# Kernel optimization log

Hardware: AMD Instinct MI355X
Metric: run time of the kernel (lower is better)

## Reference

```python
import jax, jax.numpy as jnp
import numpy as np

K = 7      # kernel_size
PAD = 3    # padding ('same' with stride 1)
G = 16     # groups


def _unfold(x):
    """torch nn.Unfold equivalent, stride=1, dilation=1.
    Returns [B, C, K*K, H, W] with kernel positions ordered (kh, kw),
    matching torch's (c, kh, kw) channel-major layout after reshape."""
    B, C, H, W = x.shape
    xp = jnp.pad(x, ((0, 0), (0, 0), (PAD, PAD), (PAD, PAD)))
    patches = jnp.stack(
        [xp[:, :, i:i + H, j:j + W] for i in range(K) for j in range(K)],
        axis=2,
    )
    return patches


def setup_inputs() -> dict:
    key = jax.random.key(0)
    k1, k2, k3 = jax.random.split(key, 3)
    B, C, H, W = 4, 256, 64, 64
    x = jax.random.normal(k1, (B, C, H, W), dtype=jnp.float32)
    # 1x1 conv producing kernel_prod*groups = 49*16 = 784 channels (with bias)
    w_kernel = jax.random.normal(k2, (G * K * K, C), dtype=jnp.float32) * 0.05
    b_kernel = jax.random.normal(k3, (G * K * K,), dtype=jnp.float32) * 0.05
    return {"x": x, "w_kernel": w_kernel, "b_kernel": b_kernel}


def reference(x, w_kernel, b_kernel):
    B, C, H, W = x.shape
    Cg = C // G
    # unfolded input: [B, G, C//G, K*K, H, W]
    patches = _unfold(x).reshape(B, G, Cg, K * K, H, W)
    # dynamic per-pixel kernel: AvgPool(k=1) is identity at stride 1,
    # then 1x1 conv with bias -> [B, G*K*K, H, W]
    kern = jnp.einsum('bchw,kc->bkhw', x, w_kernel) + b_kernel[None, :, None, None]
    kern = kern.reshape(B, G, 1, K * K, H, W)
    # multiply and sum-reduce over kernel positions, flatten groups
    out = (patches * kern).sum(axis=3).reshape(B, C, H, W)
    return out
```

## Files before the change

kernel.cpp:

```cpp
#include <hip/hip_runtime.h>


#define B_   4
#define C_   256
#define G_   16
#define KK_  49
#define KS_  7
#define PD_  3

#define PROW  70
#define POCT  (PROW*PROW)
#define XP8_BYTES (B_*32*POCT*16)
#define WBF_OFF   XP8_BYTES

#define SKW   28

typedef __attribute__((ext_vector_type(8))) short bf16x8;
typedef __attribute__((ext_vector_type(4))) float f32x4;
typedef unsigned short ushort_t;

__device__ inline unsigned f2bf(float f) {
    unsigned u = __float_as_uint(f);
    u += 0x7FFF + ((u >> 16) & 1);
    return u >> 16;
}

__global__ __launch_bounds__(256)
void cvt_xp8(const float* __restrict__ x, const float* __restrict__ wk,
             ushort_t* __restrict__ xp8, unsigned* __restrict__ wbf) {
    const int t = threadIdx.x;
    if (blockIdx.x == 64) {
        const int slice = blockIdx.z * 4 + blockIdx.y;
        const float2* wk2 = (const float2*)wk;
        const int base = slice * 6272;
        for (int k = t; k < 6272; k += 256) {
            float2 v = wk2[base + k];
            wbf[base + k] = f2bf(v.x) | (f2bf(v.y) << 16);
        }
        return;
    }
    if (blockIdx.x == 65) {
        const int b  = blockIdx.z;
        const int o0 = blockIdx.y * 8;
        const uint4 z = make_uint4(0u, 0u, 0u, 0u);
        #pragma unroll
        for (int o = 0; o < 8; ++o) {
            ushort_t* base = xp8 + (size_t)((b << 5) + o0 + o) * POCT * 8;
            for (int e = t; e < 804; e += 256) {
                int row, col;
                if (e < 420) {
                    row = e / 70; col = e - row * 70;
                    if (row >= 3) row += 64;
                } else {
                    int f = e - 420;
                    row = 3 + f / 6;
                    int m = f - (f / 6) * 6;
                    col = (m < 3) ? m : 64 + m;
                }
                *(uint4*)(base + (row * PROW + col) * 8) = z;
            }
        }
        return;
    }
    __shared__ float tile[64][65];
    const int p0 = blockIdx.x * 64;
    const int c0 = blockIdx.y * 64;
    const int b  = blockIdx.z;
    const int px_r = t & 63;
    #pragma unroll
    for (int i = 0; i < 16; ++i) {
        int ch = (t >> 6) + i * 4;
        tile[ch][px_r] = x[((size_t)(b * C_ + c0 + ch) << 12) + p0 + px_r];
    }
    __syncthreads();
    const int px = t & 63;
    const int ob = t >> 6;
    #pragma unroll
    for (int jj = 0; jj < 2; ++jj) {
        const int j = ob + jj * 4;
        unsigned u[4];
        #pragma unroll
        for (int k2 = 0; k2 < 4; ++k2) {
            float a0 = tile[j * 8 + 2 * k2][px];
            float a1 = tile[j * 8 + 2 * k2 + 1][px];
            u[k2] = f2bf(a0) | (f2bf(a1) << 16);
        }
        ushort_t* dst = xp8 + ((size_t)((b << 5) + (c0 >> 3) + j) * POCT
                               + (blockIdx.x + 3) * PROW + 3 + px) * 8;
        *(uint4*)dst = make_uint4(u[0], u[1], u[2], u[3]);
    }
}

__global__ __launch_bounds__(512, 8)
void inv_fused(const ushort_t* __restrict__ xp8,
               const ushort_t* __restrict__ wbf,
               const float* __restrict__ bk,
               float* __restrict__ out) {
    __shared__ unsigned kern2[256 * SKW];

    const int bid  = blockIdx.x;
    const int g    = bid >> 6;
    const int b    = (bid >> 4) & 3;
    const int tile = bid & 15;
    const int gy0  = tile * 4;
    const int p0   = tile * 256;

    const int tid  = threadIdx.x;
    const int wv   = tid >> 6;
    const int ln15 = tid & 15;
    const int quad = (tid & 63) >> 4;

    f32x4 acc[8];
    #pragma unroll
    for (int i = 0; i < 8; ++i) acc[i] = (f32x4){0.f, 0.f, 0.f, 0.f};

    const char* bbase = (const char*)xp8 + (size_t)b * 32 * POCT * 16;
    const char* abase = (const char*)wbf + (size_t)g * KK_ * 512;

    int vb0, vb1;
    {
        int gi0 = p0 + wv * 32 + ln15;
        int gi1 = gi0 + 16;
        vb0 = (quad * POCT + ((gi0 >> 6) + 3) * PROW + 3 + (gi0 & 63)) * 16;
        vb1 = (quad * POCT + ((gi1 >> 6) + 3) * PROW + 3 + (gi1 & 63)) * 16;
    }
    int va  = ln15 * 512 + quad * 16;
    int va3 = 48 * 512 + quad * 16;

    #pragma unroll
    for (int k = 0; k < 8; ++k) {
        bf16x8 af0 = *(const bf16x8*)(abase + va);
        bf16x8 af1 = *(const bf16x8*)(abase + 8192 + va);
        bf16x8 af2 = *(const bf16x8*)(abase + 16384 + va);
        bf16x8 af3 = *(const bf16x8*)(abase + va3);
        bf16x8 bf0 = *(const bf16x8*)(bbase + vb0);
        bf16x8 bf1 = *(const bf16x8*)(bbase + vb1);
        acc[0] = __builtin_amdgcn_mfma_f32_16x16x32_bf16(af0, bf0, acc[0], 0, 0, 0);
        acc[1] = __builtin_amdgcn_mfma_f32_16x16x32_bf16(af0, bf1, acc[1], 0, 0, 0);
        acc[2] = __builtin_amdgcn_mfma_f32_16x16x32_bf16(af1, bf0, acc[2], 0, 0, 0);
        acc[3] = __builtin_amdgcn_mfma_f32_16x16x32_bf16(af1, bf1, acc[3], 0, 0, 0);
        acc[4] = __builtin_amdgcn_mfma_f32_16x16x32_bf16(af2, bf0, acc[4], 0, 0, 0);
        acc[5] = __builtin_amdgcn_mfma_f32_16x16x32_bf16(af2, bf1, acc[5], 0, 0, 0);
        acc[6] = __builtin_amdgcn_mfma_f32_16x16x32_bf16(af3, bf0, acc[6], 0, 0, 0);
        acc[7] = __builtin_amdgcn_mfma_f32_16x16x32_bf16(af3, bf1, acc[7], 0, 0, 0);
        va  += 64;  va3 += 64;
        vb0 += 4 * POCT * 16; vb1 += 4 * POCT * 16;
    }

    #pragma unroll
    for (int mt = 0; mt < 3; ++mt) {
        const int m0 = mt * 16 + quad * 4;
        const float b0 = bk[g * KK_ + m0],     b1 = bk[g * KK_ + m0 + 1];
        const float b2 = bk[g * KK_ + m0 + 2], b3 = bk[g * KK_ + m0 + 3];
        #pragma unroll
        for (int nt = 0; nt < 2; ++nt) {
            const int p = wv * 32 + nt * 16 + ln15;
            uint2 d;
            d.x = f2bf(acc[mt * 2 + nt][0] + b0) | (f2bf(acc[mt * 2 + nt][1] + b1) << 16);
            d.y = f2bf(acc[mt * 2 + nt][2] + b2) | (f2bf(acc[mt * 2 + nt][3] + b3) << 16);
            *(uint2*)&kern2[p * SKW + mt * 8 + quad * 2] = d;
        }
    }
    if (quad == 0) {
        const float b48 = bk[g * KK_ + 48];
        #pragma unroll
        for (int nt = 0; nt < 2; ++nt) {
            const int p = wv * 32 + nt * 16 + ln15;
            kern2[p * SKW + 24] = f2bf(acc[6 + nt][0] + b48);
        }
    }

    __syncthreads();

    const int pix = tid & 255;
    const int ho  = tid >> 8;
    unsigned kd[28];
    {
        const uint4* kr = (const uint4*)&kern2[pix * SKW];
        #pragma unroll
        for (int q = 0; q < 7; ++q) {
            uint4 h = kr[q];
            kd[4*q] = h.x; kd[4*q+1] = h.y; kd[4*q+2] = h.z; kd[4*q+3] = h.w;
        }
    }

    const int py = pix >> 6, px = pix & 63;
    int vh = ((2 * g + ho) * POCT + (gy0 + py) * PROW + px) * 16;

    float a[8];
    #pragma unroll
    for (int q = 0; q < 8; ++q) a[q] = 0.f;
    #pragma unroll
    for (int kh = 0; kh < KS_; ++kh) {
        #pragma unroll
        for (int kw = 0; kw < KS_; ++kw) {
            uint4 hv = *(const uint4*)(bbase + vh + kw * 16);
            const int t49 = kh * KS_ + kw;
            unsigned d = kd[t49 >> 1];
            float kk = __uint_as_float((t49 & 1) ? (d & 0xffff0000u) : (d << 16));
            a[0] = fmaf(__uint_as_float(hv.x << 16), kk, a[0]);
            a[1] = fmaf(__uint_as_float(hv.x),       kk, a[1]);
            a[2] = fmaf(__uint_as_float(hv.y << 16), kk, a[2]);
            a[3] = fmaf(__uint_as_float(hv.y),       kk, a[3]);
            a[4] = fmaf(__uint_as_float(hv.z << 16), kk, a[4]);
            a[5] = fmaf(__uint_as_float(hv.z),       kk, a[5]);
            a[6] = fmaf(__uint_as_float(hv.w << 16), kk, a[6]);
            a[7] = fmaf(__uint_as_float(hv.w),       kk, a[7]);
        }
        vh += PROW * 16;
    }
    const size_t o = ((size_t)(b * C_ + g * 16 + ho * 8) << 12) + p0 + pix;
    #pragma unroll
    for (int q = 0; q < 8; ++q)
        out[o + ((size_t)q << 12)] = a[q];
}

extern "C" void kernel_launch(void* const* d_in, const int* in_sizes, int n_in,
                              void* d_out, int out_size, void* d_ws, size_t ws_size,
                              hipStream_t stream) {
    const float* x  = (const float*)d_in[0];
    const float* wk = (const float*)d_in[1];
    const float* bk = (const float*)d_in[2];
    float* o = (float*)d_out;

    ushort_t* xp8 = (ushort_t*)d_ws;
    unsigned* wbf = (unsigned*)((char*)d_ws + WBF_OFF);

    cvt_xp8<<<dim3(66, 4, B_), dim3(256), 0, stream>>>(x, wk, xp8, wbf);
    inv_fused<<<dim3(1024), dim3(512), 0, stream>>>(
        xp8, (const ushort_t*)wbf, bk, o);
}
```

Measured before the change: 117.7 us.

## Stage input halo tile in LDS and pad rows to 72 for aligned access

The second phase now reads its 10x70 halo window of bf16 channel octets from a shared-memory tile rather than issuing 49 global loads per thread. The halo loads are issued before the kernel-weight epilogue so their latency is hidden behind it, and the same LDS buffer is reused after an extra barrier. The kernel-weight LDS layout becomes plane-major to avoid bank conflicts, padded rows grow from 70 to 72 elements, and the conversion kernel writes the left/right padding columns inline. This costs an extra synchronization and more complex index math in exchange for less global/L2 traffic.

Result: faster. 114.0 us (-3.1%).

```diff
diff --git a/kernel.cpp b/kernel.cpp
--- a/kernel.cpp
+++ b/kernel.cpp
@@ -8,12 +8,10 @@
 #define KS_  7
 #define PD_  3
 
-#define PROW  70
-#define POCT  (PROW*PROW)
+#define PROW  72
+#define POCT  (70*PROW)
 #define XP8_BYTES (B_*32*POCT*16)
 #define WBF_OFF   XP8_BYTES
-
-#define SKW   28
 
 typedef __attribute__((ext_vector_type(8))) short bf16x8;
 typedef __attribute__((ext_vector_type(4))) float f32x4;
@@ -43,51 +41,52 @@
         const int b  = blockIdx.z;
         const int o0 = blockIdx.y * 8;
         const uint4 z = make_uint4(0u, 0u, 0u, 0u);
-        #pragma unroll
-        for (int o = 0; o < 8; ++o) {
-            ushort_t* base = xp8 + (size_t)((b << 5) + o0 + o) * POCT * 8;
-            for (int e = t; e < 804; e += 256) {
-                int row, col;
-                if (e < 420) {
-                    row = e / 70; col = e - row * 70;
-                    if (row >= 3) row += 64;
-                } else {
-                    int f = e - 420;
-                    row = 3 + f / 6;
-                    int m = f - (f / 6) * 6;
-                    col = (m < 3) ? m : 64 + m;
-                }
-                *(uint4*)(base + (row * PROW + col) * 8) = z;
-            }
+        for (int e = t; e < 6 * PROW * 8; e += 256) {
+            const int o = e / (6 * PROW);
+            const int f = e - o * (6 * PROW);
+            const int r = f / PROW;
+            const int c = f - r * PROW;
+            const int row = (r < 3) ? r : 64 + r;
+            *(uint4*)(xp8 + ((size_t)((b << 5) + o0 + o) * POCT + row * PROW + c) * 8) = z;
         }
         return;
     }
     __shared__ float tile[64][65];
-    const int p0 = blockIdx.x * 64;
     const int c0 = blockIdx.y * 64;
     const int b  = blockIdx.z;
     const int px_r = t & 63;
     #pragma unroll
     for (int i = 0; i < 16; ++i) {
         int ch = (t >> 6) + i * 4;
-        tile[ch][px_r] = x[((size_t)(b * C_ + c0 + ch) << 12) + p0 + px_r];
-    }
-    __syncthreads();
-    const int px = t & 63;
+        tile[ch][px_r] = x[((size_t)(b * C_ + c0 + ch) << 12) + blockIdx.x * 64 + px_r];
+    }
+    __syncthreads();
+    const int lane = t & 63;
     const int ob = t >> 6;
     #pragma unroll
     for (int jj = 0; jj < 2; ++jj) {
         const int j = ob + jj * 4;
-        unsigned u[4];
-        #pragma unroll
-        for (int k2 = 0; k2 < 4; ++k2) {
-            float a0 = tile[j * 8 + 2 * k2][px];
-            float a1 = tile[j * 8 + 2 * k2 + 1][px];
-            u[k2] = f2bf(a0) | (f2bf(a1) << 16);
-        }
-        ushort_t* dst = xp8 + ((size_t)((b << 5) + (c0 >> 3) + j) * POCT
-                               + (blockIdx.x + 3) * PROW + 3 + px) * 8;
-        *(uint4*)dst = make_uint4(u[0], u[1], u[2], u[3]);
+        ushort_t* rowbase = xp8 + ((size_t)((b << 5) + (c0 >> 3) + j) * POCT
+                                   + (blockIdx.x + 3) * PROW) * 8;
+        #pragma unroll
+        for (int cc = 0; cc < 2; ++cc) {
+            const int col = lane + cc * 64;
+            if (col < PROW) {
+                uint4 v = make_uint4(0u, 0u, 0u, 0u);
+                if (col >= 3 && col < 67) {
+                    const int p = col - 3;
+                    unsigned u[4];
+                    #pragma unroll
+                    for (int k2 = 0; k2 < 4; ++k2) {
+                        float a0 = tile[j * 8 + 2 * k2][p];
+                        float a1 = tile[j * 8 + 2 * k2 + 1][p];
+                        u[k2] = f2bf(a0) | (f2bf(a1) << 16);
+                    }
+                    v = make_uint4(u[0], u[1], u[2], u[3]);
+                }
+                *(uint4*)(rowbase + col * 8) = v;
+            }
+        }
     }
 }
 
@@ -96,7 +95,7 @@
                const ushort_t* __restrict__ wbf,
                const float* __restrict__ bk,
                float* __restrict__ out) {
-    __shared__ unsigned kern2[256 * SKW];
+    __shared__ unsigned lds[7168];
 
     const int bid  = blockIdx.x;
     const int g    = bid >> 6;
@@ -125,14 +124,14 @@
         vb1 = (quad * POCT + ((gi1 >> 6) + 3) * PROW + 3 + (gi1 & 63)) * 16;
     }
     int va  = ln15 * 512 + quad * 16;
-    int va3 = 48 * 512 + quad * 16;
+    const int va3 = 48 * 512 + quad * 16;
 
     #pragma unroll
     for (int k = 0; k < 8; ++k) {
         bf16x8 af0 = *(const bf16x8*)(abase + va);
         bf16x8 af1 = *(const bf16x8*)(abase + 8192 + va);
         bf16x8 af2 = *(const bf16x8*)(abase + 16384 + va);
-        bf16x8 af3 = *(const bf16x8*)(abase + va3);
+        bf16x8 af3 = *(const bf16x8*)(abase + va3 + k * 64);
         bf16x8 bf0 = *(const bf16x8*)(bbase + vb0);
         bf16x8 bf1 = *(const bf16x8*)(bbase + vb1);
         acc[0] = __builtin_amdgcn_mfma_f32_16x16x32_bf16(af0, bf0, acc[0], 0, 0, 0);
@@ -143,22 +142,35 @@
         acc[5] = __builtin_amdgcn_mfma_f32_16x16x32_bf16(af2, bf1, acc[5], 0, 0, 0);
         acc[6] = __builtin_amdgcn_mfma_f32_16x16x32_bf16(af3, bf0, acc[6], 0, 0, 0);
         acc[7] = __builtin_amdgcn_mfma_f32_16x16x32_bf16(af3, bf1, acc[7], 0, 0, 0);
-        va  += 64;  va3 += 64;
+        va  += 64;
         vb0 += 4 * POCT * 16; vb1 += 4 * POCT * 16;
     }
+
+    #define HALO_LD(e_) ({                                                     \
+        int e = (e_);                                                          \
+        int o = (e >= 700) ? 1 : 0;                                            \
+        int f = e - o * 700;                                                   \
+        int r = f / 70;                                                        \
+        int c = f - r * 70;                                                    \
+        *(const uint4*)(bbase + ((size_t)(2 * g + o) * POCT                    \
+                                 + (gy0 + r) * PROW + c) * 16); })
+    uint4 h0 = HALO_LD(tid);
+    uint4 h1 = HALO_LD(tid + 512);
+    uint4 h2 = (tid < 376) ? HALO_LD(tid + 1024) : make_uint4(0u, 0u, 0u, 0u);
 
     #pragma unroll
     for (int mt = 0; mt < 3; ++mt) {
         const int m0 = mt * 16 + quad * 4;
         const float b0 = bk[g * KK_ + m0],     b1 = bk[g * KK_ + m0 + 1];
         const float b2 = bk[g * KK_ + m0 + 2], b3 = bk[g * KK_ + m0 + 3];
+        const int q7 = mt * 2 + (quad >> 1);
         #pragma unroll
         for (int nt = 0; nt < 2; ++nt) {
             const int p = wv * 32 + nt * 16 + ln15;
             uint2 d;
             d.x = f2bf(acc[mt * 2 + nt][0] + b0) | (f2bf(acc[mt * 2 + nt][1] + b1) << 16);
             d.y = f2bf(acc[mt * 2 + nt][2] + b2) | (f2bf(acc[mt * 2 + nt][3] + b3) << 16);
-            *(uint2*)&kern2[p * SKW + mt * 8 + quad * 2] = d;
+            *(uint2*)&lds[(q7 * 256 + p) * 4 + (quad & 1) * 2] = d;
         }
     }
     if (quad == 0) {
@@ -166,35 +178,38 @@
         #pragma unroll
         for (int nt = 0; nt < 2; ++nt) {
             const int p = wv * 32 + nt * 16 + ln15;
-            kern2[p * SKW + 24] = f2bf(acc[6 + nt][0] + b48);
-        }
-    }
-
+            lds[(6 * 256 + p) * 4] = f2bf(acc[6 + nt][0] + b48);
+        }
+    }
     __syncthreads();
 
     const int pix = tid & 255;
     const int ho  = tid >> 8;
     unsigned kd[28];
-    {
-        const uint4* kr = (const uint4*)&kern2[pix * SKW];
-        #pragma unroll
-        for (int q = 0; q < 7; ++q) {
-            uint4 h = kr[q];
-            kd[4*q] = h.x; kd[4*q+1] = h.y; kd[4*q+2] = h.z; kd[4*q+3] = h.w;
-        }
-    }
+    #pragma unroll
+    for (int q = 0; q < 7; ++q) {
+        uint4 h = *(const uint4*)&lds[(q * 256 + pix) * 4];
+        kd[4*q] = h.x; kd[4*q+1] = h.y; kd[4*q+2] = h.z; kd[4*q+3] = h.w;
+    }
+    __syncthreads();
+
+    *(uint4*)&lds[tid * 4] = h0;
+    *(uint4*)&lds[(tid + 512) * 4] = h1;
+    if (tid < 376) *(uint4*)&lds[(tid + 1024) * 4] = h2;
+    __syncthreads();
 
     const int py = pix >> 6, px = pix & 63;
-    int vh = ((2 * g + ho) * POCT + (gy0 + py) * PROW + px) * 16;
+    const int hbase = (ho * 700 + py * 70 + px) * 4;
 
     float a[8];
     #pragma unroll
     for (int q = 0; q < 8; ++q) a[q] = 0.f;
     #pragma unroll
     for (int kh = 0; kh < KS_; ++kh) {
+        const uint4* hr = (const uint4*)&lds[hbase + kh * 280];
         #pragma unroll
         for (int kw = 0; kw < KS_; ++kw) {
-            uint4 hv = *(const uint4*)(bbase + vh + kw * 16);
+            uint4 hv = hr[kw];
             const int t49 = kh * KS_ + kw;
             unsigned d = kd[t49 >> 1];
             float kk = __uint_as_float((t49 & 1) ? (d & 0xffff0000u) : (d << 16));
@@ -207,7 +222,6 @@
             a[6] = fmaf(__uint_as_float(hv.w << 16), kk, a[6]);
             a[7] = fmaf(__uint_as_float(hv.w),       kk, a[7]);
         }
-        vh += PROW * 16;
     }
     const size_t o = ((size_t)(b * C_ + g * 16 + ho * 8) << 12) + p0 + pix;
     #pragma unroll
```

## Drop padded input layout; clamp indices and mask taps in aggregation

Applied to the files above, without the earlier changes.

The bf16 channel-octet buffer becomes unpadded 64x64, so the zero-border fill blocks go away and the conversion grid shrinks. The aggregation loop now clamps source coordinates and zeroes the kernel weight for out-of-bounds taps. The shared-memory kernel-weight array is rearranged into seven 256-pixel planes so the per-pixel vector reads hit separate banks. The trade is extra min/max and select work on every tap in exchange for fewer writes and a smaller working set.

New measurement: 118.0 us. Within noise of the previous version (+0.2%).

```diff
diff --git a/kernel.cpp b/kernel.cpp
--- a/kernel.cpp
+++ b/kernel.cpp
@@ -8,12 +8,8 @@
 #define KS_  7
 #define PD_  3
 
-#define PROW  70
-#define POCT  (PROW*PROW)
-#define XP8_BYTES (B_*32*POCT*16)
+#define XP8_BYTES (B_*32*4096*8*2)
 #define WBF_OFF   XP8_BYTES
-
-#define SKW   28
 
 typedef __attribute__((ext_vector_type(8))) short bf16x8;
 typedef __attribute__((ext_vector_type(4))) float f32x4;
@@ -39,29 +35,6 @@
         }
         return;
     }
-    if (blockIdx.x == 65) {
-        const int b  = blockIdx.z;
-        const int o0 = blockIdx.y * 8;
-        const uint4 z = make_uint4(0u, 0u, 0u, 0u);
-        #pragma unroll
-        for (int o = 0; o < 8; ++o) {
-            ushort_t* base = xp8 + (size_t)((b << 5) + o0 + o) * POCT * 8;
-            for (int e = t; e < 804; e += 256) {
-                int row, col;
-                if (e < 420) {
-                    row = e / 70; col = e - row * 70;
-                    if (row >= 3) row += 64;
-                } else {
-                    int f = e - 420;
-                    row = 3 + f / 6;
-                    int m = f - (f / 6) * 6;
-                    col = (m < 3) ? m : 64 + m;
-                }
-                *(uint4*)(base + (row * PROW + col) * 8) = z;
-            }
-        }
-        return;
-    }
     __shared__ float tile[64][65];
     const int p0 = blockIdx.x * 64;
     const int c0 = blockIdx.y * 64;
@@ -85,8 +58,7 @@
             float a1 = tile[j * 8 + 2 * k2 + 1][px];
             u[k2] = f2bf(a0) | (f2bf(a1) << 16);
         }
-        ushort_t* dst = xp8 + ((size_t)((b << 5) + (c0 >> 3) + j) * POCT
-                               + (blockIdx.x + 3) * PROW + 3 + px) * 8;
+        ushort_t* dst = xp8 + (((size_t)((b << 5) + (c0 >> 3) + j) << 12) + p0 + px) * 8;
         *(uint4*)dst = make_uint4(u[0], u[1], u[2], u[3]);
     }
 }
@@ -96,7 +68,7 @@
                const ushort_t* __restrict__ wbf,
                const float* __restrict__ bk,
                float* __restrict__ out) {
-    __shared__ unsigned kern2[256 * SKW];
+    __shared__ unsigned kq[7 * 256 * 4];
 
     const int bid  = blockIdx.x;
     const int g    = bid >> 6;
@@ -114,25 +86,24 @@
     #pragma unroll
     for (int i = 0; i < 8; ++i) acc[i] = (f32x4){0.f, 0.f, 0.f, 0.f};
 
-    const char* bbase = (const char*)xp8 + (size_t)b * 32 * POCT * 16;
+    const char* bbase = (const char*)xp8 + ((size_t)b << 21);
     const char* abase = (const char*)wbf + (size_t)g * KK_ * 512;
 
-    int vb0, vb1;
+    int vb0;
     {
         int gi0 = p0 + wv * 32 + ln15;
-        int gi1 = gi0 + 16;
-        vb0 = (quad * POCT + ((gi0 >> 6) + 3) * PROW + 3 + (gi0 & 63)) * 16;
-        vb1 = (quad * POCT + ((gi1 >> 6) + 3) * PROW + 3 + (gi1 & 63)) * 16;
-    }
+        vb0 = ((quad << 12) + gi0) << 4;
+    }
+    int vb1 = vb0 + 256;
     int va  = ln15 * 512 + quad * 16;
-    int va3 = 48 * 512 + quad * 16;
+    const int va3 = 48 * 512 + quad * 16;
 
     #pragma unroll
     for (int k = 0; k < 8; ++k) {
         bf16x8 af0 = *(const bf16x8*)(abase + va);
         bf16x8 af1 = *(const bf16x8*)(abase + 8192 + va);
         bf16x8 af2 = *(const bf16x8*)(abase + 16384 + va);
-        bf16x8 af3 = *(const bf16x8*)(abase + va3);
+        bf16x8 af3 = *(const bf16x8*)(abase + va3 + k * 64);
         bf16x8 bf0 = *(const bf16x8*)(bbase + vb0);
         bf16x8 bf1 = *(const bf16x8*)(bbase + vb1);
         acc[0] = __builtin_amdgcn_mfma_f32_16x16x32_bf16(af0, bf0, acc[0], 0, 0, 0);
@@ -143,8 +114,8 @@
         acc[5] = __builtin_amdgcn_mfma_f32_16x16x32_bf16(af2, bf1, acc[5], 0, 0, 0);
         acc[6] = __builtin_amdgcn_mfma_f32_16x16x32_bf16(af3, bf0, acc[6], 0, 0, 0);
         acc[7] = __builtin_amdgcn_mfma_f32_16x16x32_bf16(af3, bf1, acc[7], 0, 0, 0);
-        va  += 64;  va3 += 64;
-        vb0 += 4 * POCT * 16; vb1 += 4 * POCT * 16;
+        va  += 64;
+        vb0 += 4 * 4096 * 16; vb1 += 4 * 4096 * 16;
     }
 
     #pragma unroll
@@ -152,13 +123,14 @@
         const int m0 = mt * 16 + quad * 4;
         const float b0 = bk[g * KK_ + m0],     b1 = bk[g * KK_ + m0 + 1];
         const float b2 = bk[g * KK_ + m0 + 2], b3 = bk[g * KK_ + m0 + 3];
+        const int q7 = mt * 2 + (quad >> 1);
         #pragma unroll
         for (int nt = 0; nt < 2; ++nt) {
             const int p = wv * 32 + nt * 16 + ln15;
             uint2 d;
             d.x = f2bf(acc[mt * 2 + nt][0] + b0) | (f2bf(acc[mt * 2 + nt][1] + b1) << 16);
             d.y = f2bf(acc[mt * 2 + nt][2] + b2) | (f2bf(acc[mt * 2 + nt][3] + b3) << 16);
-            *(uint2*)&kern2[p * SKW + mt * 8 + quad * 2] = d;
+            *(uint2*)&kq[(q7 * 256 + p) * 4 + (quad & 1) * 2] = d;
         }
     }
     if (quad == 0) {
@@ -166,38 +138,41 @@
         #pragma unroll
         for (int nt = 0; nt < 2; ++nt) {
             const int p = wv * 32 + nt * 16 + ln15;
-            kern2[p * SKW + 24] = f2bf(acc[6 + nt][0] + b48);
-        }
-    }
-
+            kq[(6 * 256 + p) * 4] = f2bf(acc[6 + nt][0] + b48);
+        }
+    }
     __syncthreads();
 
     const int pix = tid & 255;
     const int ho  = tid >> 8;
     unsigned kd[28];
-    {
-        const uint4* kr = (const uint4*)&kern2[pix * SKW];
-        #pragma unroll
-        for (int q = 0; q < 7; ++q) {
-            uint4 h = kr[q];
-            kd[4*q] = h.x; kd[4*q+1] = h.y; kd[4*q+2] = h.z; kd[4*q+3] = h.w;
-        }
-    }
-
-    const int py = pix >> 6, px = pix & 63;
-    int vh = ((2 * g + ho) * POCT + (gy0 + py) * PROW + px) * 16;
+    #pragma unroll
+    for (int q = 0; q < 7; ++q) {
+        uint4 h = *(const uint4*)&kq[(q * 256 + pix) * 4];
+        kd[4*q] = h.x; kd[4*q+1] = h.y; kd[4*q+2] = h.z; kd[4*q+3] = h.w;
+    }
+
+    const int py = pix >> 6, pxx = pix & 63;
+    const char* obse = (const char*)xp8 + ((size_t)((b << 5) + 2 * g + ho) << 16);
 
     float a[8];
     #pragma unroll
     for (int q = 0; q < 8; ++q) a[q] = 0.f;
     #pragma unroll
     for (int kh = 0; kh < KS_; ++kh) {
+        const int sy  = gy0 + py + kh - PD_;
+        const int csy = min(max(sy, 0), 63);
+        const bool oky = (sy == csy);
+        const char* hrow = obse + ((size_t)csy << 10);
         #pragma unroll
         for (int kw = 0; kw < KS_; ++kw) {
-            uint4 hv = *(const uint4*)(bbase + vh + kw * 16);
+            const int sx  = pxx + kw - PD_;
+            const int csx = min(max(sx, 0), 63);
+            uint4 hv = *(const uint4*)(hrow + (csx << 4));
             const int t49 = kh * KS_ + kw;
             unsigned d = kd[t49 >> 1];
             float kk = __uint_as_float((t49 & 1) ? (d & 0xffff0000u) : (d << 16));
+            kk = (oky && sx == csx) ? kk : 0.f;
             a[0] = fmaf(__uint_as_float(hv.x << 16), kk, a[0]);
             a[1] = fmaf(__uint_as_float(hv.x),       kk, a[1]);
             a[2] = fmaf(__uint_as_float(hv.y << 16), kk, a[2]);
@@ -207,7 +182,6 @@
             a[6] = fmaf(__uint_as_float(hv.w << 16), kk, a[6]);
             a[7] = fmaf(__uint_as_float(hv.w),       kk, a[7]);
         }
-        vh += PROW * 16;
     }
     const size_t o = ((size_t)(b * C_ + g * 16 + ho * 8) << 12) + p0 + pix;
     #pragma unroll
@@ -226,7 +200,7 @@
     ushort_t* xp8 = (ushort_t*)d_ws;
     unsigned* wbf = (unsigned*)((char*)d_ws + WBF_OFF);
 
-    cvt_xp8<<<dim3(66, 4, B_), dim3(256), 0, stream>>>(x, wk, xp8, wbf);
+    cvt_xp8<<<dim3(65, 4, B_), dim3(256), 0, stream>>>(x, wk, xp8, wbf);
     inv_fused<<<dim3(1024), dim3(512), 0, stream>>>(
         xp8, (const ushort_t*)wbf, bk, o);
 }
```
